# Kernel optimization log

Hardware: AMD Instinct MI355X
Metric: run time of the kernel (lower is better)

The kernel has to match this reference:

```python
import jax, jax.numpy as jnp
import numpy as np

H, W = 4096, 4096

# Fixed tiny kernels expressed as shifted-slice sums (exactly equivalent to
# F.conv2d with stride=1, padding=0 for these 0/1 kernels).

def _diag(x):   # [[1,0],[0,1]] -> (H-1, W-1)
    return x[:-1, :-1] + x[1:, 1:]

def _anti(x):   # [[0,1],[1,0]]
    return x[:-1, 1:] + x[1:, :-1]

def _all2(x):   # 2x2 all-ones
    return x[:-1, :-1] + x[:-1, 1:] + x[1:, :-1] + x[1:, 1:]

def _cross(x):  # 3x3 plus-shape -> (H-2, W-2)
    return x[:-2, 1:-1] + x[2:, 1:-1] + x[1:-1, :-2] + x[1:-1, 2:]

def setup_inputs() -> dict:
    key = jax.random.key(0)
    board = jax.random.randint(key, (H, W), 0, 3, dtype=jnp.int32)
    return {"board_np": board}

def reference(board_np):
    black = (board_np == 1).astype(jnp.float32)
    white = (board_np == 2).astype(jnp.float32)
    empty = (board_np == 0).astype(jnp.float32)

    black_diag, black_anti = _diag(black), _anti(black)
    white_diag, white_anti = _diag(white), _anti(white)
    empty_diag, empty_anti = _diag(empty), _anti(empty)

    bamboo_black = ((black_diag == 2) & (empty_anti == 2)) | ((black_anti == 2) & (empty_diag == 2))
    bamboo_white = ((white_diag == 2) & (empty_anti == 2)) | ((white_anti == 2) & (empty_diag == 2))

    black_s2, white_s2, empty_s2 = _all2(black), _all2(white), _all2(empty)
    # tmp_de/ae/be/ce: single-cell picks of the 2x2 window
    empty_d = empty[1:, 1:]
    empty_a = empty[:-1, :-1]
    empty_b = empty[:-1, 1:]
    empty_c = empty[1:, :-1]
    any_empty_corner = (empty_d == 1) | (empty_a == 1) | (empty_b == 1) | (empty_c == 1)

    tiger_black = (black_s2 >= 2) & any_empty_corner
    tiger_white = (white_s2 >= 2) & any_empty_corner
    empty_triangle_black = (black_s2 == 3) & (empty_s2 == 1)
    empty_triangle_white = (white_s2 == 3) & (empty_s2 == 1)

    empty_center = empty[1:-1, 1:-1]  # k_center conv
    eye_black = (empty_center == 1) & (_cross(black) == 4)
    eye_white = (empty_center == 1) & (_cross(white) == 4)

    return (bamboo_black, bamboo_white, tiger_black, tiger_white,
            empty_triangle_black, empty_triangle_white, eye_black, eye_white)
```

## Files before the change

kernel.cpp:

```cpp
#include <hip/hip_runtime.h>


#define BW   4096
#define W1   4095
#define W2   4094

__global__ __launch_bounds__(256)
void motif_kernel(const int* __restrict__ board, int* __restrict__ out) {
    const int j = blockIdx.x * 256 + threadIdx.x;
    const int i = blockIdx.y;
    if (j >= W1) return;

    const int* row0 = board + i * BW;
    const int* row1 = row0 + BW;

    const int a = row0[j];
    const int b = row0[j + 1];
    const int c = row1[j];
    const int d = row1[j + 1];

    const int nb_d = (a == 1) + (d == 1);
    const int nb_a = (b == 1) + (c == 1);
    const int nw_d = (a == 2) + (d == 2);
    const int nw_a = (b == 2) + (c == 2);
    const int ne_d = (a == 0) + (d == 0);
    const int ne_a = (b == 0) + (c == 0);

    const int nb = nb_d + nb_a;
    const int nw = nw_d + nw_a;
    const int ne = ne_d + ne_a;

    const bool bamboo_b = ((nb_d == 2) & (ne_a == 2)) | ((nb_a == 2) & (ne_d == 2));
    const bool bamboo_w = ((nw_d == 2) & (ne_a == 2)) | ((nw_a == 2) & (ne_d == 2));
    const bool any_empty = ne >= 1;
    const bool tiger_b = (nb >= 2) & any_empty;
    const bool tiger_w = (nw >= 2) & any_empty;
    const bool et_b = (nb == 3) & (ne == 1);
    const bool et_w = (nw == 3) & (ne == 1);

    const int N1 = W1 * W1;
    const int o  = i * W1 + j;
    out[o]           = (int)bamboo_b;
    out[N1 + o]      = (int)bamboo_w;
    out[2 * N1 + o]  = (int)tiger_b;
    out[3 * N1 + o]  = (int)tiger_w;
    out[4 * N1 + o]  = (int)et_b;
    out[5 * N1 + o]  = (int)et_w;

    if ((i < W2) & (j < W2)) {
        const int dn = board[(i + 2) * BW + (j + 1)];
        const int rt = row1[j + 2];
        const bool eye_b = (d == 0) & (b == 1) & (c == 1) & (dn == 1) & (rt == 1);
        const bool eye_w = (d == 0) & (b == 2) & (c == 2) & (dn == 2) & (rt == 2);
        const int o2 = 6 * N1 + i * W2 + j;
        out[o2]            = (int)eye_b;
        out[o2 + W2 * W2]  = (int)eye_w;
    }
}

extern "C" void kernel_launch(void* const* d_in, const int* in_sizes, int n_in,
                              void* d_out, int out_size, void* d_ws, size_t ws_size,
                              hipStream_t stream) {
    const int* board = (const int*)d_in[0];
    int* out = (int*)d_out;

    dim3 block(256, 1, 1);
    dim3 grid((W1 + 255) / 256, W1, 1);
    motif_kernel<<<grid, block, 0, stream>>>(board, out);
}
```

Before: 632.4 us.

## Process 4 columns × 8 rows per thread with vector loads and rolling row reuse

Each thread now handles four adjacent columns and walks down eight rows, keeping a rolling three-row register window so each board row is loaded once per thread rather than redundantly. Loads use 16-byte plus 8-byte vector reads and the six motif outputs plus two eye outputs are written as 4-wide vector stores, which may be unaligned because row pitch W1 is odd. This cuts the load instruction count and redundant reads in what is a write-bandwidth-bound kernel. It also reduces the grid to far fewer blocks, which lowers parallelism per block.

Result: faster. 612.6 us (-3.1%).

```diff
diff --git a/kernel.cpp b/kernel.cpp
--- a/kernel.cpp
+++ b/kernel.cpp
@@ -4,57 +4,100 @@
 #define BW   4096
 #define W1   4095
 #define W2   4094
+#define ROWS 8
+
+typedef int i4u __attribute__((vector_size(16), aligned(4)));
+typedef int i4a __attribute__((vector_size(16), aligned(16)));
+typedef int i2a __attribute__((vector_size(8),  aligned(8)));
 
 __global__ __launch_bounds__(256)
 void motif_kernel(const int* __restrict__ board, int* __restrict__ out) {
-    const int j = blockIdx.x * 256 + threadIdx.x;
-    const int i = blockIdx.y;
-    if (j >= W1) return;
+    const int t  = blockIdx.x * 256 + threadIdx.x;
+    const int j0 = t << 2;
+    const int i0 = blockIdx.y * ROWS;
+    const bool tailj = (j0 == BW - 4);
 
-    const int* row0 = board + i * BW;
-    const int* row1 = row0 + BW;
+    int c0[6], c1[6], c2[6];
 
-    const int a = row0[j];
-    const int b = row0[j + 1];
-    const int c = row1[j];
-    const int d = row1[j + 1];
+    const int* rp = board + (size_t)i0 * BW + j0;
 
-    const int nb_d = (a == 1) + (d == 1);
-    const int nb_a = (b == 1) + (c == 1);
-    const int nw_d = (a == 2) + (d == 2);
-    const int nw_a = (b == 2) + (c == 2);
-    const int ne_d = (a == 0) + (d == 0);
-    const int ne_a = (b == 0) + (c == 0);
+    auto load6 = [&](const int* p, int* w) {
+        i4a v = *(const i4a*)p;
+        w[0] = v[0]; w[1] = v[1]; w[2] = v[2]; w[3] = v[3];
+        if (!tailj) { i2a u = *(const i2a*)(p + 4); w[4] = u[0]; w[5] = u[1]; }
+        else        { w[4] = 0; w[5] = 0; }
+    };
 
-    const int nb = nb_d + nb_a;
-    const int nw = nw_d + nw_a;
-    const int ne = ne_d + ne_a;
-
-    const bool bamboo_b = ((nb_d == 2) & (ne_a == 2)) | ((nb_a == 2) & (ne_d == 2));
-    const bool bamboo_w = ((nw_d == 2) & (ne_a == 2)) | ((nw_a == 2) & (ne_d == 2));
-    const bool any_empty = ne >= 1;
-    const bool tiger_b = (nb >= 2) & any_empty;
-    const bool tiger_w = (nw >= 2) & any_empty;
-    const bool et_b = (nb == 3) & (ne == 1);
-    const bool et_w = (nw == 3) & (ne == 1);
+    load6(rp, c0);
+    load6(rp + BW, c1);
 
     const int N1 = W1 * W1;
-    const int o  = i * W1 + j;
-    out[o]           = (int)bamboo_b;
-    out[N1 + o]      = (int)bamboo_w;
-    out[2 * N1 + o]  = (int)tiger_b;
-    out[3 * N1 + o]  = (int)tiger_w;
-    out[4 * N1 + o]  = (int)et_b;
-    out[5 * N1 + o]  = (int)et_w;
+    const int N2 = W2 * W2;
 
-    if ((i < W2) & (j < W2)) {
-        const int dn = board[(i + 2) * BW + (j + 1)];
-        const int rt = row1[j + 2];
-        const bool eye_b = (d == 0) & (b == 1) & (c == 1) & (dn == 1) & (rt == 1);
-        const bool eye_w = (d == 0) & (b == 2) & (c == 2) & (dn == 2) & (rt == 2);
-        const int o2 = 6 * N1 + i * W2 + j;
-        out[o2]            = (int)eye_b;
-        out[o2 + W2 * W2]  = (int)eye_w;
+    #pragma unroll
+    for (int r = 0; r < ROWS; ++r) {
+        const int i = i0 + r;
+        if (i >= W1) break;
+        if (i + 2 < BW)
+            load6(board + (size_t)(i + 2) * BW + j0, c2);
+
+        int vb[4], vw[4], vtb[4], vtw[4], veb[4], vew[4], eb[4], ew[4];
+        #pragma unroll
+        for (int k = 0; k < 4; ++k) {
+            const int a = c0[k], b = c0[k + 1], c = c1[k], d = c1[k + 1];
+            const int nb_d = (a == 1) + (d == 1), nb_a = (b == 1) + (c == 1);
+            const int nw_d = (a == 2) + (d == 2), nw_a = (b == 2) + (c == 2);
+            const int ne_d = (a == 0) + (d == 0), ne_a = (b == 0) + (c == 0);
+            const int nb = nb_d + nb_a, nw = nw_d + nw_a, ne = ne_d + ne_a;
+            vb[k]  = (int)(((nb_d == 2) & (ne_a == 2)) | ((nb_a == 2) & (ne_d == 2)));
+            vw[k]  = (int)(((nw_d == 2) & (ne_a == 2)) | ((nw_a == 2) & (ne_d == 2)));
+            const int anyE = (int)(ne >= 1);
+            vtb[k] = ((int)(nb >= 2)) & anyE;
+            vtw[k] = ((int)(nw >= 2)) & anyE;
+            veb[k] = (int)((nb == 3) & (ne == 1));
+            vew[k] = (int)((nw == 3) & (ne == 1));
+            const int dn = c2[k + 1], rt = c1[k + 2];
+            eb[k] = (int)((d == 0) & (b == 1) & (c == 1) & (dn == 1) & (rt == 1));
+            ew[k] = (int)((d == 0) & (b == 2) & (c == 2) & (dn == 2) & (rt == 2));
+        }
+
+        const int o = i * W1 + j0;
+        if (!tailj) {
+            i4u s;
+            s[0]=vb[0];  s[1]=vb[1];  s[2]=vb[2];  s[3]=vb[3];  *(i4u*)(out + o)          = s;
+            s[0]=vw[0];  s[1]=vw[1];  s[2]=vw[2];  s[3]=vw[3];  *(i4u*)(out + o + N1)     = s;
+            s[0]=vtb[0]; s[1]=vtb[1]; s[2]=vtb[2]; s[3]=vtb[3]; *(i4u*)(out + o + 2*N1)   = s;
+            s[0]=vtw[0]; s[1]=vtw[1]; s[2]=vtw[2]; s[3]=vtw[3]; *(i4u*)(out + o + 3*N1)   = s;
+            s[0]=veb[0]; s[1]=veb[1]; s[2]=veb[2]; s[3]=veb[3]; *(i4u*)(out + o + 4*N1)   = s;
+            s[0]=vew[0]; s[1]=vew[1]; s[2]=vew[2]; s[3]=vew[3]; *(i4u*)(out + o + 5*N1)   = s;
+        } else {
+            #pragma unroll
+            for (int k = 0; k < 3; ++k) {
+                out[o + k]          = vb[k];
+                out[o + k + N1]     = vw[k];
+                out[o + k + 2*N1]   = vtb[k];
+                out[o + k + 3*N1]   = vtw[k];
+                out[o + k + 4*N1]   = veb[k];
+                out[o + k + 5*N1]   = vew[k];
+            }
+        }
+
+        if (i < W2) {
+            const int o2 = 6 * N1 + i * W2 + j0;
+            if (!tailj) {
+                i4u s;
+                s[0]=eb[0]; s[1]=eb[1]; s[2]=eb[2]; s[3]=eb[3]; *(i4u*)(out + o2)      = s;
+                s[0]=ew[0]; s[1]=ew[1]; s[2]=ew[2]; s[3]=ew[3]; *(i4u*)(out + o2 + N2) = s;
+            } else {
+                out[o2]          = eb[0];
+                out[o2 + 1]      = eb[1];
+                out[o2 + N2]     = ew[0];
+                out[o2 + N2 + 1] = ew[1];
+            }
+        }
+
+        #pragma unroll
+        for (int q = 0; q < 6; ++q) { c0[q] = c1[q]; c1[q] = c2[q]; }
     }
 }
 
@@ -65,6 +108,6 @@
     int* out = (int*)d_out;
 
     dim3 block(256, 1, 1);
-    dim3 grid((W1 + 255) / 256, W1, 1);
+    dim3 grid(4, (W1 + ROWS - 1) / ROWS, 1);
     motif_kernel<<<grid, block, 0, stream>>>(board, out);
 }
```

## Vectorize motif kernel to four cells per thread with aligned 16-byte stores

Applied to the files above, without the earlier changes.

Each thread now computes four adjacent output columns from 16-byte vector loads of three board rows, packing the motif flags into bitmasks. Stores to each output plane are realigned per row (the plane row stride is 4095 or 4094, so alignment shifts with i mod 4) so they can be issued as aligned 16-byte vector stores, with scalar stores for the edge columns. This cuts load and store instruction counts for a memory-bound kernel that writes eight output planes. The cost is more complex indexing, templated store paths and more registers per thread.

Result: faster. 599.0 us (-5.3%).

```diff
diff --git a/kernel.cpp b/kernel.cpp
--- a/kernel.cpp
+++ b/kernel.cpp
@@ -1,60 +1,134 @@
 #include <hip/hip_runtime.h>
 
 
-#define BW   4096
-#define W1   4095
-#define W2   4094
+#define BW 4096
+#define W1 4095
+#define W2 4094
+#define N1 16769025
+#define N2 16760836
+
+typedef int i4a __attribute__((vector_size(16), aligned(16)));
+
+template<int IM4>
+__device__ __forceinline__ void store_planes(
+    int* __restrict__ out, const int i, const int u, const bool has2,
+    const int (&cellm)[7], const int (&eyem)[6])
+{
+    const bool fullv = (u < 1023);
+    const size_t orow = (size_t)i * W1 + (u << 2);
+
+    #pragma unroll
+    for (int p = 0; p < 6; ++p) {
+        const int sp = (IM4 - p) & 3;
+        int* dst = out + (size_t)p * N1 + orow;
+        if (fullv) {
+            i4a s;
+            s[0] = (cellm[sp + 0] >> p) & 1;
+            s[1] = (cellm[sp + 1] >> p) & 1;
+            s[2] = (cellm[sp + 2] >> p) & 1;
+            s[3] = (cellm[sp + 3] >> p) & 1;
+            *(i4a*)(dst + sp) = s;
+        } else {
+            #pragma unroll
+            for (int k = 0; k < 3 - sp; ++k)
+                dst[sp + k] = (cellm[sp + k] >> p) & 1;
+        }
+        if (u == 0) {
+            #pragma unroll
+            for (int k = 0; k < sp; ++k)
+                dst[k] = (cellm[k] >> p) & 1;
+        }
+    }
+
+    if (has2) {
+        const int e = (IM4 & 1) ? 0 : 2;
+        int* d0 = out + (size_t)6 * N1 + (size_t)i * W2 + (u << 2);
+        int* d1 = d0 + N2;
+        if (fullv) {
+            i4a s0, s1;
+            #pragma unroll
+            for (int k = 0; k < 4; ++k) {
+                s0[k] =  eyem[e + k]       & 1;
+                s1[k] = (eyem[e + k] >> 1) & 1;
+            }
+            *(i4a*)(d0 + e) = s0;
+            *(i4a*)(d1 + e) = s1;
+        } else if (e == 0) {
+            #pragma unroll
+            for (int k = 0; k < 2; ++k) {
+                d0[k] =  eyem[k]       & 1;
+                d1[k] = (eyem[k] >> 1) & 1;
+            }
+        }
+        if (u == 0) {
+            #pragma unroll
+            for (int k = 0; k < e; ++k) {
+                d0[k] =  eyem[k]       & 1;
+                d1[k] = (eyem[k] >> 1) & 1;
+            }
+        }
+    }
+}
 
 __global__ __launch_bounds__(256)
 void motif_kernel(const int* __restrict__ board, int* __restrict__ out) {
-    const int j = blockIdx.x * 256 + threadIdx.x;
+    const int u = blockIdx.x * 256 + threadIdx.x;
     const int i = blockIdx.y;
-    if (j >= W1) return;
+    const int base = u << 2;
+    const bool fullv = (u < 1023);
+    const bool has2  = (i < W2);
 
-    const int* row0 = board + i * BW;
-    const int* row1 = row0 + BW;
+    const int* p0 = board + (size_t)i * BW + base;
+    const int* p1 = p0 + BW;
+    const int* p2 = p1 + BW;
 
-    const int a = row0[j];
-    const int b = row0[j + 1];
-    const int c = row1[j];
-    const int d = row1[j + 1];
+    i4a a0 = *(const i4a*)p0;
+    i4a a1 = *(const i4a*)p1;
+    i4a b0 = {0, 0, 0, 0}, b1 = {0, 0, 0, 0};
+    if (fullv) { b0 = *(const i4a*)(p0 + 4); b1 = *(const i4a*)(p1 + 4); }
+    i4a a2 = {0, 0, 0, 0}, b2 = {0, 0, 0, 0};
+    if (has2) {
+        a2 = *(const i4a*)p2;
+        if (fullv) b2 = *(const i4a*)(p2 + 4);
+    }
 
-    const int nb_d = (a == 1) + (d == 1);
-    const int nb_a = (b == 1) + (c == 1);
-    const int nw_d = (a == 2) + (d == 2);
-    const int nw_a = (b == 2) + (c == 2);
-    const int ne_d = (a == 0) + (d == 0);
-    const int ne_a = (b == 0) + (c == 0);
+    const int r0[8] = {a0[0], a0[1], a0[2], a0[3], b0[0], b0[1], b0[2], b0[3]};
+    const int r1[8] = {a1[0], a1[1], a1[2], a1[3], b1[0], b1[1], b1[2], b1[3]};
+    const int r2[8] = {a2[0], a2[1], a2[2], a2[3], b2[0], b2[1], b2[2], b2[3]};
 
-    const int nb = nb_d + nb_a;
-    const int nw = nw_d + nw_a;
-    const int ne = ne_d + ne_a;
+    int cellm[7];
+    #pragma unroll
+    for (int p = 0; p < 7; ++p) {
+        const int a = r0[p], b = r0[p + 1], c = r1[p], d = r1[p + 1];
+        const int nb_d = (a == 1) + (d == 1), nb_a = (b == 1) + (c == 1);
+        const int nw_d = (a == 2) + (d == 2), nw_a = (b == 2) + (c == 2);
+        const int ne_d = (a == 0) + (d == 0), ne_a = (b == 0) + (c == 0);
+        const int nb = nb_d + nb_a, nw = nw_d + nw_a, ne = ne_d + ne_a;
+        const int bb  = ((nb_d == 2) & (ne_a == 2)) | ((nb_a == 2) & (ne_d == 2));
+        const int bw_ = ((nw_d == 2) & (ne_a == 2)) | ((nw_a == 2) & (ne_d == 2));
+        const int anyE = (ne >= 1);
+        const int tb = (nb >= 2) & anyE;
+        const int tw = (nw >= 2) & anyE;
+        const int eb = (nb == 3) & (ne == 1);
+        const int ew = (nw == 3) & (ne == 1);
+        cellm[p] = bb | (bw_ << 1) | (tb << 2) | (tw << 3) | (eb << 4) | (ew << 5);
+    }
 
-    const bool bamboo_b = ((nb_d == 2) & (ne_a == 2)) | ((nb_a == 2) & (ne_d == 2));
-    const bool bamboo_w = ((nw_d == 2) & (ne_a == 2)) | ((nw_a == 2) & (ne_d == 2));
-    const bool any_empty = ne >= 1;
-    const bool tiger_b = (nb >= 2) & any_empty;
-    const bool tiger_w = (nw >= 2) & any_empty;
-    const bool et_b = (nb == 3) & (ne == 1);
-    const bool et_w = (nw == 3) & (ne == 1);
+    int eyem[6];
+    #pragma unroll
+    for (int q = 0; q < 6; ++q) {
+        const int ce = r1[q + 1], up = r0[q + 1], lf = r1[q],
+                  dn = r2[q + 1], rt = r1[q + 2];
+        const int eB = (ce == 0) & (up == 1) & (lf == 1) & (dn == 1) & (rt == 1);
+        const int eW = (ce == 0) & (up == 2) & (lf == 2) & (dn == 2) & (rt == 2);
+        eyem[q] = eB | (eW << 1);
+    }
 
-    const int N1 = W1 * W1;
-    const int o  = i * W1 + j;
-    out[o]           = (int)bamboo_b;
-    out[N1 + o]      = (int)bamboo_w;
-    out[2 * N1 + o]  = (int)tiger_b;
-    out[3 * N1 + o]  = (int)tiger_w;
-    out[4 * N1 + o]  = (int)et_b;
-    out[5 * N1 + o]  = (int)et_w;
-
-    if ((i < W2) & (j < W2)) {
-        const int dn = board[(i + 2) * BW + (j + 1)];
-        const int rt = row1[j + 2];
-        const bool eye_b = (d == 0) & (b == 1) & (c == 1) & (dn == 1) & (rt == 1);
-        const bool eye_w = (d == 0) & (b == 2) & (c == 2) & (dn == 2) & (rt == 2);
-        const int o2 = 6 * N1 + i * W2 + j;
-        out[o2]            = (int)eye_b;
-        out[o2 + W2 * W2]  = (int)eye_w;
+    switch (i & 3) {
+        case 0: store_planes<0>(out, i, u, has2, cellm, eyem); break;
+        case 1: store_planes<1>(out, i, u, has2, cellm, eyem); break;
+        case 2: store_planes<2>(out, i, u, has2, cellm, eyem); break;
+        case 3: store_planes<3>(out, i, u, has2, cellm, eyem); break;
     }
 }
 
@@ -65,6 +139,6 @@
     int* out = (int*)d_out;
 
     dim3 block(256, 1, 1);
-    dim3 grid((W1 + 255) / 256, W1, 1);
+    dim3 grid(4, W1, 1);
     motif_kernel<<<grid, block, 0, stream>>>(board, out);
 }
```

## Use wavefront ballot bitmasks with vertical row strips to compute motifs

Applied to the files above, without the earlier changes.

Each 64-lane wavefront handles a 63-column band across a strip of 15 rows. Board rows are turned into black/white bitmasks via __ballot and kept in a 3-row rolling buffer, so each row is read once per band instead of up to four times per output cell. All motifs are then evaluated with 64-bit bitwise logic. This lowers redundant global reads and ALU work, but output writes (about 8 int arrays) still dominate traffic, and the 64-thread blocks with a 63-wide stride leave one lane idle and give store rows a slightly misaligned start.

New measurement: 693.3 us. 9.6% more time.

```diff
diff --git a/kernel.cpp b/kernel.cpp
--- a/kernel.cpp
+++ b/kernel.cpp
@@ -1,60 +1,85 @@
 #include <hip/hip_runtime.h>
+#include <cstdint>
 
 
-#define BW   4096
-#define W1   4095
-#define W2   4094
+#define BW 4096
+#define W1 4095
+#define W2 4094
+#define N1 16769025ULL
+#define N2 16760836ULL
+#define RSTRIP 15
 
-__global__ __launch_bounds__(256)
+__global__ __launch_bounds__(64)
 void motif_kernel(const int* __restrict__ board, int* __restrict__ out) {
-    const int j = blockIdx.x * 256 + threadIdx.x;
-    const int i = blockIdx.y;
-    if (j >= W1) return;
+    const int lane = threadIdx.x;
+    const int band = blockIdx.x;
+    const int i0   = blockIdx.y * RSTRIP;
+    const int col  = band * 63 + lane;
+    const int colh = (col < W1) ? col + 1 : W1;
 
-    const int* row0 = board + i * BW;
-    const int* row1 = row0 + BW;
+    uint64_t Bl[3], Bh[3], Wl[3], Wh[3];
 
-    const int a = row0[j];
-    const int b = row0[j + 1];
-    const int c = row1[j];
-    const int d = row1[j + 1];
+    auto load_row = [&](int row, int s) {
+        const int* p = board + (size_t)row * BW;
+        const int vlo = p[col];
+        const int vhi = p[colh];
+        Bl[s] = __ballot(vlo == 1);
+        Wl[s] = __ballot(vlo == 2);
+        Bh[s] = __ballot(vhi == 1);
+        Wh[s] = __ballot(vhi == 2);
+    };
 
-    const int nb_d = (a == 1) + (d == 1);
-    const int nb_a = (b == 1) + (c == 1);
-    const int nw_d = (a == 2) + (d == 2);
-    const int nw_a = (b == 2) + (c == 2);
-    const int ne_d = (a == 0) + (d == 0);
-    const int ne_a = (b == 0) + (c == 0);
+    load_row(i0, 0);
+    load_row(i0 + 1, 1);
 
-    const int nb = nb_d + nb_a;
-    const int nw = nw_d + nw_a;
-    const int ne = ne_d + ne_a;
+    const bool cellStore = (lane < 63);
+    const bool eyeColOk  = cellStore && (col < W2);
 
-    const bool bamboo_b = ((nb_d == 2) & (ne_a == 2)) | ((nb_a == 2) & (ne_d == 2));
-    const bool bamboo_w = ((nw_d == 2) & (ne_a == 2)) | ((nw_a == 2) & (ne_d == 2));
-    const bool any_empty = ne >= 1;
-    const bool tiger_b = (nb >= 2) & any_empty;
-    const bool tiger_w = (nw >= 2) & any_empty;
-    const bool et_b = (nb == 3) & (ne == 1);
-    const bool et_w = (nw == 3) & (ne == 1);
+    #pragma unroll 3
+    for (int r = 0; r < RSTRIP; ++r) {
+        const int i  = i0 + r;
+        const int s0 = r % 3, s1 = (r + 1) % 3, s2 = (r + 2) % 3;
 
-    const int N1 = W1 * W1;
-    const int o  = i * W1 + j;
-    out[o]           = (int)bamboo_b;
-    out[N1 + o]      = (int)bamboo_w;
-    out[2 * N1 + o]  = (int)tiger_b;
-    out[3 * N1 + o]  = (int)tiger_w;
-    out[4 * N1 + o]  = (int)et_b;
-    out[5 * N1 + o]  = (int)et_w;
+        int rowLoad = i + 2;
+        if (rowLoad > W1) rowLoad = W1;
+        load_row(rowLoad, s2);
 
-    if ((i < W2) & (j < W2)) {
-        const int dn = board[(i + 2) * BW + (j + 1)];
-        const int rt = row1[j + 2];
-        const bool eye_b = (d == 0) & (b == 1) & (c == 1) & (dn == 1) & (rt == 1);
-        const bool eye_w = (d == 0) & (b == 2) & (c == 2) & (dn == 2) & (rt == 2);
-        const int o2 = 6 * N1 + i * W2 + j;
-        out[o2]            = (int)eye_b;
-        out[o2 + W2 * W2]  = (int)eye_w;
+        const uint64_t Ba = Bl[s0], Bb = Bh[s0], Bc = Bl[s1], Bd = Bh[s1];
+        const uint64_t Wa = Wl[s0], Wb = Wh[s0], Wc = Wl[s1], Wd = Wh[s1];
+        const uint64_t Ea = ~(Ba | Wa);
+        const uint64_t Eb = ~(Bb | Wb);
+        const uint64_t Ec = ~(Bc | Wc);
+        const uint64_t Ed = ~(Bd | Wd);
+
+        const uint64_t bamboo_b = (Ba & Bd & Eb & Ec) | (Bb & Bc & Ea & Ed);
+        const uint64_t bamboo_w = (Wa & Wd & Eb & Ec) | (Wb & Wc & Ea & Ed);
+
+        const uint64_t anyE = Ea | Eb | Ec | Ed;
+        const uint64_t tb2 = (Ba&Bb)|(Ba&Bc)|(Ba&Bd)|(Bb&Bc)|(Bb&Bd)|(Bc&Bd);
+        const uint64_t tw2 = (Wa&Wb)|(Wa&Wc)|(Wa&Wd)|(Wb&Wc)|(Wb&Wd)|(Wc&Wd);
+        const uint64_t tiger_b = tb2 & anyE;
+        const uint64_t tiger_w = tw2 & anyE;
+
+        const uint64_t etri_b = (Ea&Bb&Bc&Bd)|(Ba&Eb&Bc&Bd)|(Ba&Bb&Ec&Bd)|(Ba&Bb&Bc&Ed);
+        const uint64_t etri_w = (Ea&Wb&Wc&Wd)|(Wa&Eb&Wc&Wd)|(Wa&Wb&Ec&Wd)|(Wa&Wb&Wc&Ed);
+
+        const uint64_t eye_b = Ed & Bb & Bc & (Bd >> 1) & Bh[s2];
+        const uint64_t eye_w = Ed & Wb & Wc & (Wd >> 1) & Wh[s2];
+
+        const size_t orow = (size_t)i * W1 + col;
+        if (cellStore) {
+            out[orow]            = (int)((bamboo_b >> lane) & 1);
+            out[orow + N1]       = (int)((bamboo_w >> lane) & 1);
+            out[orow + 2 * N1]   = (int)((tiger_b  >> lane) & 1);
+            out[orow + 3 * N1]   = (int)((tiger_w  >> lane) & 1);
+            out[orow + 4 * N1]   = (int)((etri_b   >> lane) & 1);
+            out[orow + 5 * N1]   = (int)((etri_w   >> lane) & 1);
+        }
+        if (eyeColOk && (i < W2)) {
+            const size_t oeye = 6 * N1 + (size_t)i * W2 + col;
+            out[oeye]      = (int)((eye_b >> lane) & 1);
+            out[oeye + N2] = (int)((eye_w >> lane) & 1);
+        }
     }
 }
 
@@ -64,7 +89,7 @@
     const int* board = (const int*)d_in[0];
     int* out = (int*)d_out;
 
-    dim3 block(256, 1, 1);
-    dim3 grid((W1 + 255) / 256, W1, 1);
+    dim3 block(64, 1, 1);
+    dim3 grid(65, 273, 1);
     motif_kernel<<<grid, block, 0, stream>>>(board, out);
 }
```
